# Optimization experiments

Hardware: AMD Instinct MI355X
Metric: run time of the kernel (lower is better)

Reference implementation:

```python
import jax, jax.numpy as jnp
import numpy as np

N = 50000
E = 800000
D = 96

def setup_inputs() -> dict:
    key = jax.random.key(0)
    ks = jax.random.split(key, 8)
    s = 1.0 / np.sqrt(D)
    return {
        "x": jax.random.normal(ks[0], (N, D), dtype=jnp.float32),
        "edge_index": jax.random.randint(ks[1], (2, E), 0, N, dtype=jnp.int64),
        "Wl1": jax.random.normal(ks[2], (D, D), dtype=jnp.float32) * s,
        "bl1": jnp.zeros((D,), dtype=jnp.float32),
        "Wr1": jax.random.normal(ks[3], (D, D), dtype=jnp.float32) * s,
        "Wl2": jax.random.normal(ks[4], (D, D), dtype=jnp.float32) * s,
        "bl2": jnp.zeros((D,), dtype=jnp.float32),
        "Wr2": jax.random.normal(ks[5], (D, D), dtype=jnp.float32) * s,
    }

def _mean_aggr(h, src, dst, num_nodes):
    # gather source features, segment-sum into targets, divide by in-degree
    msgs = h[src]                                         # [E, D]
    summed = jax.ops.segment_sum(msgs, dst, num_segments=num_nodes)  # [N, D]
    deg = jax.ops.segment_sum(jnp.ones((src.shape[0],), h.dtype), dst,
                              num_segments=num_nodes)     # [N]
    return summed / jnp.maximum(deg, 1.0)[:, None]

def _sage_conv(h, src, dst, Wl, bl, Wr, num_nodes):
    agg = _mean_aggr(h, src, dst, num_nodes)
    # out = lin_l(mean_aggr) + lin_r(x)
    return agg @ Wl.T + bl + h @ Wr.T

def reference(x, edge_index, Wl1, bl1, Wr1, Wl2, bl2, Wr2):
    src, dst = edge_index[0], edge_index[1]
    n = x.shape[0]
    h = _sage_conv(x, src, dst, Wl1, bl1, Wr1, n)
    h = jax.nn.relu(h)
    h = _sage_conv(h, src, dst, Wl2, bl2, Wr2, n)
    return h
```

## Files before the change

### kernel.cpp

```cpp
#include <hip/hip_runtime.h>
#include <hip/hip_bf16.h>

#define D 96
#define DQ 24
#define KS_PAD 104

typedef _Float16 half8 __attribute__((ext_vector_type(8)));
typedef float floatx4 __attribute__((ext_vector_type(4)));

__global__ __launch_bounds__(256) void hist_kernel(const int* __restrict__ dst,
                                                   int* __restrict__ cnt, int E) {
    int e = blockIdx.x * 256 + threadIdx.x;
    if (e < E) atomicAdd(&cnt[dst[e]], 1);
}

__global__ __launch_bounds__(1024) void scan1_kernel(const int* __restrict__ cnt,
                                                     int* __restrict__ rs,
                                                     int* __restrict__ bsum, int n) {
    __shared__ int buf[1024];
    int t = threadIdx.x;
    int gid = blockIdx.x * 1024 + t;
    int v = (gid < n) ? cnt[gid] : 0;
    buf[t] = v;
    __syncthreads();
    for (int off = 1; off < 1024; off <<= 1) {
        int u = (t >= off) ? buf[t - off] : 0;
        __syncthreads();
        buf[t] += u;
        __syncthreads();
    }
    if (gid < n) rs[gid] = buf[t] - v;
    if (t == 1023) bsum[blockIdx.x] = buf[1023];
}

__global__ __launch_bounds__(64) void scan2_kernel(const int* __restrict__ bsum,
                                                   int* __restrict__ boff, int nb,
                                                   int* __restrict__ rs, int n) {
    __shared__ int buf[64];
    int t = threadIdx.x;
    int v = (t < nb) ? bsum[t] : 0;
    buf[t] = v;
    __syncthreads();
    for (int off = 1; off < 64; off <<= 1) {
        int u = (t >= off) ? buf[t - off] : 0;
        __syncthreads();
        buf[t] += u;
        __syncthreads();
    }
    if (t < nb) boff[t] = buf[t] - v;
    if (t == 63) rs[n] = buf[63];
}

__global__ __launch_bounds__(1024) void scan3_kernel(int* __restrict__ rs,
                                                     const int* __restrict__ boff, int n) {
    int gid = blockIdx.x * 1024 + threadIdx.x;
    if (gid < n) rs[gid] += boff[blockIdx.x];
}

__global__ __launch_bounds__(256) void fill_kernel(const int* __restrict__ src,
                                                   const int* __restrict__ dst,
                                                   const int* __restrict__ rs,
                                                   int* __restrict__ cur,
                                                   int* __restrict__ col, int E) {
    int e = blockIdx.x * 256 + threadIdx.x;
    if (e < E) {
        int d = dst[e];
        int pos = rs[d] + atomicAdd(&cur[d], 1);
        col[pos] = src[e];
    }
}

__global__ __launch_bounds__(256) void aggregate_kernel(const float* __restrict__ h,
                                                        const int* __restrict__ rs,
                                                        const int* __restrict__ col,
                                                        float* __restrict__ agg, int n) {
    int idx = blockIdx.x * 256 + threadIdx.x;
    if (idx >= n * DQ) return;
    int node = idx / DQ;
    int q = idx - node * DQ;
    int beg = rs[node], end = rs[node + 1];
    float ax0=0.f, ay0=0.f, az0=0.f, aw0=0.f;
    float ax1=0.f, ay1=0.f, az1=0.f, aw1=0.f;
    float ax2=0.f, ay2=0.f, az2=0.f, aw2=0.f;
    float ax3=0.f, ay3=0.f, az3=0.f, aw3=0.f;
    int i = beg;
    for (; i + 4 <= end; i += 4) {
        int s0 = col[i], s1 = col[i+1], s2 = col[i+2], s3 = col[i+3];
        const float4 v0 = *(const float4*)(h + (size_t)s0 * D + q * 4);
        const float4 v1 = *(const float4*)(h + (size_t)s1 * D + q * 4);
        const float4 v2 = *(const float4*)(h + (size_t)s2 * D + q * 4);
        const float4 v3 = *(const float4*)(h + (size_t)s3 * D + q * 4);
        ax0 += v0.x; ay0 += v0.y; az0 += v0.z; aw0 += v0.w;
        ax1 += v1.x; ay1 += v1.y; az1 += v1.z; aw1 += v1.w;
        ax2 += v2.x; ay2 += v2.y; az2 += v2.z; aw2 += v2.w;
        ax3 += v3.x; ay3 += v3.y; az3 += v3.z; aw3 += v3.w;
    }
    for (; i < end; ++i) {
        int s0 = col[i];
        const float4 v0 = *(const float4*)(h + (size_t)s0 * D + q * 4);
        ax0 += v0.x; ay0 += v0.y; az0 += v0.z; aw0 += v0.w;
    }
    float inv = 1.0f / fmaxf((float)(end - beg), 1.0f);
    float4 o;
    o.x = (ax0 + ax1 + ax2 + ax3) * inv;
    o.y = (ay0 + ay1 + ay2 + ay3) * inv;
    o.z = (az0 + az1 + az2 + az3) * inv;
    o.w = (aw0 + aw1 + aw2 + aw3) * inv;
    *(float4*)(agg + (size_t)node * D + q * 4) = o;
}

__global__ __launch_bounds__(256) void sage_gemm_mfma(const float* __restrict__ agg,
                                                      const float* __restrict__ hin,
                                                      const float* __restrict__ Wl,
                                                      const float* __restrict__ bl,
                                                      const float* __restrict__ Wr,
                                                      float* __restrict__ out,
                                                      int n, int relu) {
    __shared__ _Float16 swl[96 * KS_PAD];
    __shared__ _Float16 swr[96 * KS_PAD];

    int tid = threadIdx.x;
    for (int i = tid; i < 96 * 96; i += 256) {
        int o = i / 96, k = i - o * 96;
        swl[o * KS_PAD + k] = (_Float16)Wl[i];
        swr[o * KS_PAD + k] = (_Float16)Wr[i];
    }
    __syncthreads();

    int lane = tid & 63;
    int w = tid >> 6;
    int m = lane & 15;
    int g = lane >> 4;

    int arow = blockIdx.x * 64 + w * 16 + m;
    int rload = (arow < n) ? arow : (n - 1);

    half8 af[3], xf[3];
    #pragma unroll
    for (int ks = 0; ks < 3; ++ks) {
        const float* pa = agg + (size_t)rload * D + ks * 32 + g * 8;
        const float* px = hin + (size_t)rload * D + ks * 32 + g * 8;
        float4 a0 = *(const float4*)pa;
        float4 a1 = *(const float4*)(pa + 4);
        float4 x0 = *(const float4*)px;
        float4 x1 = *(const float4*)(px + 4);
        af[ks] = (half8){(_Float16)a0.x, (_Float16)a0.y, (_Float16)a0.z, (_Float16)a0.w,
                         (_Float16)a1.x, (_Float16)a1.y, (_Float16)a1.z, (_Float16)a1.w};
        xf[ks] = (half8){(_Float16)x0.x, (_Float16)x0.y, (_Float16)x0.z, (_Float16)x0.w,
                         (_Float16)x1.x, (_Float16)x1.y, (_Float16)x1.z, (_Float16)x1.w};
    }

    int row0 = blockIdx.x * 64 + w * 16 + g * 4;
    #pragma unroll
    for (int ct = 0; ct < 6; ++ct) {
        int o = ct * 16 + m;
        floatx4 acc = {0.f, 0.f, 0.f, 0.f};
        #pragma unroll
        for (int ks = 0; ks < 3; ++ks) {
            half8 bwl = *(const half8*)&swl[o * KS_PAD + ks * 32 + g * 8];
            acc = __builtin_amdgcn_mfma_f32_16x16x32_f16(af[ks], bwl, acc, 0, 0, 0);
            half8 bwr = *(const half8*)&swr[o * KS_PAD + ks * 32 + g * 8];
            acc = __builtin_amdgcn_mfma_f32_16x16x32_f16(xf[ks], bwr, acc, 0, 0, 0);
        }
        float b = bl[o];
        #pragma unroll
        for (int p = 0; p < 4; ++p) {
            int orow = row0 + p;
            float v = acc[p] + b;
            if (relu) v = fmaxf(v, 0.f);
            if (orow < n) out[(size_t)orow * D + o] = v;
        }
    }
}

extern "C" void kernel_launch(void* const* d_in, const int* in_sizes, int n_in,
                              void* d_out, int out_size, void* d_ws, size_t ws_size,
                              hipStream_t stream) {
    const float* x   = (const float*)d_in[0];
    const int*   ei  = (const int*)d_in[1];
    const float* Wl1 = (const float*)d_in[2];
    const float* bl1 = (const float*)d_in[3];
    const float* Wr1 = (const float*)d_in[4];
    const float* Wl2 = (const float*)d_in[5];
    const float* bl2 = (const float*)d_in[6];
    const float* Wr2 = (const float*)d_in[7];
    float* out = (float*)d_out;

    int N = in_sizes[0] / D;
    int E = in_sizes[1] / 2;
    const int* src = ei;
    const int* dst = ei + E;

    char* ws = (char*)d_ws;
    float* agg = (float*)ws;
    float* h1  = agg + (size_t)N * D;
    int*   rs  = (int*)(h1 + (size_t)N * D);
    int*   cnt = rs + (N + 1);
    int*   cur = cnt + N;
    int*   col = cur + N;
    int*   bsum = col + E;
    int*   boff = bsum + 64;

    hipMemsetAsync(cnt, 0, (size_t)2 * N * sizeof(int), stream);

    int eb = (E + 255) / 256;
    int nbk = (N + 1023) / 1024;
    hist_kernel<<<eb, 256, 0, stream>>>(dst, cnt, E);
    scan1_kernel<<<nbk, 1024, 0, stream>>>(cnt, rs, bsum, N);
    scan2_kernel<<<1, 64, 0, stream>>>(bsum, boff, nbk, rs, N);
    scan3_kernel<<<nbk, 1024, 0, stream>>>(rs, boff, N);
    fill_kernel<<<eb, 256, 0, stream>>>(src, dst, rs, cur, col, E);

    int ab = (N * DQ + 255) / 256;
    int gb = (N + 63) / 64;

    aggregate_kernel<<<ab, 256, 0, stream>>>(x, rs, col, agg, N);
    sage_gemm_mfma<<<gb, 256, 0, stream>>>(agg, x, Wl1, bl1, Wr1, h1, N, 1);

    aggregate_kernel<<<ab, 256, 0, stream>>>(h1, rs, col, agg, N);
    sage_gemm_mfma<<<gb, 256, 0, stream>>>(agg, h1, Wl2, bl2, Wr2, out, N, 0);
}
```

Measured before the change: 288.1 us.

## Store node features and aggregates in fp16 to halve gather traffic

Adds a conversion kernel that turns x into fp16 and changes the aggregation and GEMM kernels to read and write fp16 intermediates (h1, agg). Each gather in the aggregation then moves 16 bytes of 8 halves per thread instead of 4 floats, which halves the random-access memory traffic. It also folds the CSR row-start offset into the cursor array inside scan3, so fill needs one atomic and no extra rs load. The cost is an extra conversion pass over x and lower precision in the stored intermediates; accumulation stays in fp32.

```diff
diff --git a/kernel.cpp b/kernel.cpp
--- a/kernel.cpp
+++ b/kernel.cpp
@@ -2,11 +2,22 @@
 #include <hip/hip_bf16.h>
 
 #define D 96
-#define DQ 24
+#define DQH 12
 #define KS_PAD 104
 
 typedef _Float16 half8 __attribute__((ext_vector_type(8)));
+typedef _Float16 half4 __attribute__((ext_vector_type(4)));
 typedef float floatx4 __attribute__((ext_vector_type(4)));
+
+__global__ __launch_bounds__(256) void cvt_kernel(const float* __restrict__ in,
+                                                  _Float16* __restrict__ out, int n4) {
+    int i = blockIdx.x * 256 + threadIdx.x;
+    if (i < n4) {
+        float4 v = ((const float4*)in)[i];
+        half4 o = { (_Float16)v.x, (_Float16)v.y, (_Float16)v.z, (_Float16)v.w };
+        ((half4*)out)[i] = o;
+    }
+}
 
 __global__ __launch_bounds__(256) void hist_kernel(const int* __restrict__ dst,
                                                    int* __restrict__ cnt, int E) {
@@ -52,69 +63,71 @@
 }
 
 __global__ __launch_bounds__(1024) void scan3_kernel(int* __restrict__ rs,
+                                                     int* __restrict__ cur,
                                                      const int* __restrict__ boff, int n) {
     int gid = blockIdx.x * 1024 + threadIdx.x;
-    if (gid < n) rs[gid] += boff[blockIdx.x];
+    if (gid < n) {
+        int v = rs[gid] + boff[blockIdx.x];
+        rs[gid] = v;
+        cur[gid] = v;
+    }
 }
 
 __global__ __launch_bounds__(256) void fill_kernel(const int* __restrict__ src,
                                                    const int* __restrict__ dst,
-                                                   const int* __restrict__ rs,
                                                    int* __restrict__ cur,
                                                    int* __restrict__ col, int E) {
     int e = blockIdx.x * 256 + threadIdx.x;
     if (e < E) {
-        int d = dst[e];
-        int pos = rs[d] + atomicAdd(&cur[d], 1);
+        int pos = atomicAdd(&cur[dst[e]], 1);
         col[pos] = src[e];
     }
 }
 
-__global__ __launch_bounds__(256) void aggregate_kernel(const float* __restrict__ h,
-                                                        const int* __restrict__ rs,
-                                                        const int* __restrict__ col,
-                                                        float* __restrict__ agg, int n) {
+__global__ __launch_bounds__(256) void aggregate_f16(const _Float16* __restrict__ h,
+                                                     const int* __restrict__ rs,
+                                                     const int* __restrict__ col,
+                                                     _Float16* __restrict__ agg, int n) {
     int idx = blockIdx.x * 256 + threadIdx.x;
-    if (idx >= n * DQ) return;
-    int node = idx / DQ;
-    int q = idx - node * DQ;
+    if (idx >= n * DQH) return;
+    int node = idx / DQH;
+    int q = idx - node * DQH;
     int beg = rs[node], end = rs[node + 1];
-    float ax0=0.f, ay0=0.f, az0=0.f, aw0=0.f;
-    float ax1=0.f, ay1=0.f, az1=0.f, aw1=0.f;
-    float ax2=0.f, ay2=0.f, az2=0.f, aw2=0.f;
-    float ax3=0.f, ay3=0.f, az3=0.f, aw3=0.f;
+    float a0[8] = {0,0,0,0,0,0,0,0}, a1[8] = {0,0,0,0,0,0,0,0};
+    float a2[8] = {0,0,0,0,0,0,0,0}, a3[8] = {0,0,0,0,0,0,0,0};
     int i = beg;
     for (; i + 4 <= end; i += 4) {
         int s0 = col[i], s1 = col[i+1], s2 = col[i+2], s3 = col[i+3];
-        const float4 v0 = *(const float4*)(h + (size_t)s0 * D + q * 4);
-        const float4 v1 = *(const float4*)(h + (size_t)s1 * D + q * 4);
-        const float4 v2 = *(const float4*)(h + (size_t)s2 * D + q * 4);
-        const float4 v3 = *(const float4*)(h + (size_t)s3 * D + q * 4);
-        ax0 += v0.x; ay0 += v0.y; az0 += v0.z; aw0 += v0.w;
-        ax1 += v1.x; ay1 += v1.y; az1 += v1.z; aw1 += v1.w;
-        ax2 += v2.x; ay2 += v2.y; az2 += v2.z; aw2 += v2.w;
-        ax3 += v3.x; ay3 += v3.y; az3 += v3.z; aw3 += v3.w;
+        half8 v0 = *(const half8*)(h + (size_t)s0 * D + q * 8);
+        half8 v1 = *(const half8*)(h + (size_t)s1 * D + q * 8);
+        half8 v2 = *(const half8*)(h + (size_t)s2 * D + q * 8);
+        half8 v3 = *(const half8*)(h + (size_t)s3 * D + q * 8);
+        #pragma unroll
+        for (int j = 0; j < 8; ++j) {
+            a0[j] += (float)v0[j]; a1[j] += (float)v1[j];
+            a2[j] += (float)v2[j]; a3[j] += (float)v3[j];
+        }
     }
     for (; i < end; ++i) {
         int s0 = col[i];
-        const float4 v0 = *(const float4*)(h + (size_t)s0 * D + q * 4);
-        ax0 += v0.x; ay0 += v0.y; az0 += v0.z; aw0 += v0.w;
+        half8 v0 = *(const half8*)(h + (size_t)s0 * D + q * 8);
+        #pragma unroll
+        for (int j = 0; j < 8; ++j) a0[j] += (float)v0[j];
     }
     float inv = 1.0f / fmaxf((float)(end - beg), 1.0f);
-    float4 o;
-    o.x = (ax0 + ax1 + ax2 + ax3) * inv;
-    o.y = (ay0 + ay1 + ay2 + ay3) * inv;
-    o.z = (az0 + az1 + az2 + az3) * inv;
-    o.w = (aw0 + aw1 + aw2 + aw3) * inv;
-    *(float4*)(agg + (size_t)node * D + q * 4) = o;
-}
-
-__global__ __launch_bounds__(256) void sage_gemm_mfma(const float* __restrict__ agg,
-                                                      const float* __restrict__ hin,
+    half8 o;
+    #pragma unroll
+    for (int j = 0; j < 8; ++j) o[j] = (_Float16)((a0[j] + a1[j] + a2[j] + a3[j]) * inv);
+    *(half8*)(agg + (size_t)node * D + q * 8) = o;
+}
+
+__global__ __launch_bounds__(256) void sage_gemm_mfma(const _Float16* __restrict__ agg,
+                                                      const _Float16* __restrict__ hin,
                                                       const float* __restrict__ Wl,
                                                       const float* __restrict__ bl,
                                                       const float* __restrict__ Wr,
-                                                      float* __restrict__ out,
+                                                      _Float16* __restrict__ out16,
+                                                      float* __restrict__ out32,
                                                       int n, int relu) {
     __shared__ _Float16 swl[96 * KS_PAD];
     __shared__ _Float16 swr[96 * KS_PAD];
@@ -138,16 +151,8 @@
     half8 af[3], xf[3];
     #pragma unroll
     for (int ks = 0; ks < 3; ++ks) {
-        const float* pa = agg + (size_t)rload * D + ks * 32 + g * 8;
-        const float* px = hin + (size_t)rload * D + ks * 32 + g * 8;
-        float4 a0 = *(const float4*)pa;
-        float4 a1 = *(const float4*)(pa + 4);
-        float4 x0 = *(const float4*)px;
-        float4 x1 = *(const float4*)(px + 4);
-        af[ks] = (half8){(_Float16)a0.x, (_Float16)a0.y, (_Float16)a0.z, (_Float16)a0.w,
-                         (_Float16)a1.x, (_Float16)a1.y, (_Float16)a1.z, (_Float16)a1.w};
-        xf[ks] = (half8){(_Float16)x0.x, (_Float16)x0.y, (_Float16)x0.z, (_Float16)x0.w,
-                         (_Float16)x1.x, (_Float16)x1.y, (_Float16)x1.z, (_Float16)x1.w};
+        af[ks] = *(const half8*)(agg + (size_t)rload * D + ks * 32 + g * 8);
+        xf[ks] = *(const half8*)(hin + (size_t)rload * D + ks * 32 + g * 8);
     }
 
     int row0 = blockIdx.x * 64 + w * 16 + g * 4;
@@ -157,10 +162,10 @@
         floatx4 acc = {0.f, 0.f, 0.f, 0.f};
         #pragma unroll
         for (int ks = 0; ks < 3; ++ks) {
-            half8 bwl = *(const half8*)&swl[o * KS_PAD + ks * 32 + g * 8];
-            acc = __builtin_amdgcn_mfma_f32_16x16x32_f16(af[ks], bwl, acc, 0, 0, 0);
-            half8 bwr = *(const half8*)&swr[o * KS_PAD + ks * 32 + g * 8];
-            acc = __builtin_amdgcn_mfma_f32_16x16x32_f16(xf[ks], bwr, acc, 0, 0, 0);
+            acc = __builtin_amdgcn_mfma_f32_16x16x32_f16(af[ks],
+                    *(const half8*)&swl[o * KS_PAD + ks * 32 + g * 8], acc, 0, 0, 0);
+            acc = __builtin_amdgcn_mfma_f32_16x16x32_f16(xf[ks],
+                    *(const half8*)&swr[o * KS_PAD + ks * 32 + g * 8], acc, 0, 0, 0);
         }
         float b = bl[o];
         #pragma unroll
@@ -168,7 +173,10 @@
             int orow = row0 + p;
             float v = acc[p] + b;
             if (relu) v = fmaxf(v, 0.f);
-            if (orow < n) out[(size_t)orow * D + o] = v;
+            if (orow < n) {
+                if (out32) out32[(size_t)orow * D + o] = v;
+                else       out16[(size_t)orow * D + o] = (_Float16)v;
+            }
         }
     }
 }
@@ -192,31 +200,35 @@
     const int* dst = ei + E;
 
     char* ws = (char*)d_ws;
-    float* agg = (float*)ws;
-    float* h1  = agg + (size_t)N * D;
-    int*   rs  = (int*)(h1 + (size_t)N * D);
-    int*   cnt = rs + (N + 1);
-    int*   cur = cnt + N;
-    int*   col = cur + N;
-    int*   bsum = col + E;
-    int*   boff = bsum + 64;
-
-    hipMemsetAsync(cnt, 0, (size_t)2 * N * sizeof(int), stream);
-
-    int eb = (E + 255) / 256;
+    _Float16* xh   = (_Float16*)ws;
+    _Float16* h1h  = xh + (size_t)N * D;
+    _Float16* aggh = h1h + (size_t)N * D;
+    int* rs   = (int*)(aggh + (size_t)N * D);
+    int* cnt  = rs + (N + 1);
+    int* cur  = cnt + N;
+    int* col  = cur + N;
+    int* bsum = col + E;
+    int* boff = bsum + 64;
+
+    hipMemsetAsync(cnt, 0, (size_t)N * sizeof(int), stream);
+
+    int eb  = (E + 255) / 256;
     int nbk = (N + 1023) / 1024;
+    int n4  = N * D / 4;
+
+    cvt_kernel<<<(n4 + 255) / 256, 256, 0, stream>>>(x, xh, n4);
     hist_kernel<<<eb, 256, 0, stream>>>(dst, cnt, E);
     scan1_kernel<<<nbk, 1024, 0, stream>>>(cnt, rs, bsum, N);
     scan2_kernel<<<1, 64, 0, stream>>>(bsum, boff, nbk, rs, N);
-    scan3_kernel<<<nbk, 1024, 0, stream>>>(rs, boff, N);
-    fill_kernel<<<eb, 256, 0, stream>>>(src, dst, rs, cur, col, E);
-
-    int ab = (N * DQ + 255) / 256;
+    scan3_kernel<<<nbk, 1024, 0, stream>>>(rs, cur, boff, N);
+    fill_kernel<<<eb, 256, 0, stream>>>(src, dst, cur, col, E);
+
+    int ab = (N * DQH + 255) / 256;
     int gb = (N + 63) / 64;
 
-    aggregate_kernel<<<ab, 256, 0, stream>>>(x, rs, col, agg, N);
-    sage_gemm_mfma<<<gb, 256, 0, stream>>>(agg, x, Wl1, bl1, Wr1, h1, N, 1);
-
-    aggregate_kernel<<<ab, 256, 0, stream>>>(h1, rs, col, agg, N);
-    sage_gemm_mfma<<<gb, 256, 0, stream>>>(agg, h1, Wl2, bl2, Wr2, out, N, 0);
-}
+    aggregate_f16<<<ab, 256, 0, stream>>>(xh, rs, col, aggh, N);
+    sage_gemm_mfma<<<gb, 256, 0, stream>>>(aggh, xh, Wl1, bl1, Wr1, h1h, nullptr, N, 1);
+
+    aggregate_f16<<<ab, 256, 0, stream>>>(h1h, rs, col, aggh, N);
+    sage_gemm_mfma<<<gb, 256, 0, stream>>>(aggh, h1h, Wl2, bl2, Wr2, nullptr, out, N, 0);
+}
```

Result: faster. 258.1 us (-10.4%).
